# Performance work log

Hardware: AMD Instinct MI355X
Metric: run time of the kernel (lower is better)

## Reference

```python
import jax, jax.numpy as jnp
import numpy as np

NUM_GRAPHS = 3000
L = 7        # num_gc_layers
D = 256      # dims * power
DIMS = 64
POWER = 4
MSG_EPS = 1e-7
LN_EPS = 1e-5


def layer_norm(x, g, b):
    mu = jnp.mean(x, axis=-1, keepdims=True)
    var = jnp.var(x, axis=-1, keepdims=True)
    return (x - mu) * jax.lax.rsqrt(var + LN_EPS) * g + b


def gen_conv(h, src, dst, edge_emb, w, b, n_nodes):
    # GENConv (OGB DeeperGCN), aggr='add', mlp_layers=1:
    #   msg = relu(x_j + e) + eps ; agg = scatter_add ; out = Linear(x + agg)
    msg = jax.nn.relu(h[src] + edge_emb) + MSG_EPS      # [E, D]
    agg = jax.ops.segment_sum(msg, dst, num_segments=n_nodes)
    return (h + agg) @ w + b


def mlp_vn(v, w1, b1, g1, be1, w2, b2, g2, be2):
    # MLP([D, D, D], norm='layer'): Lin -> LN -> ReLU -> Lin -> LN -> ReLU
    v = jax.nn.relu(layer_norm(v @ w1 + b1, g1, be1))
    v = jax.nn.relu(layer_norm(v @ w2 + b2, g2, be2))
    return v


def _forward(x, edge_attr, edge_index, batch, atom_emb, bond_emb, vn_emb,
             gcn_w, gcn_b, norm_g, norm_b, ffn_w, ffn_b,
             vn_w1, vn_b1, vn_g1, vn_be1, vn_w2, vn_b2, vn_g2, vn_be2):
    N = x.shape[0]
    # AtomEncoder / BondEncoder: sum of per-feature embedding gathers
    h = atom_emb[jnp.arange(9), x].sum(axis=1)              # [N, D]
    edge_emb = bond_emb[jnp.arange(3), edge_attr].sum(axis=1)  # [E, D]
    h_init = h

    vn = jnp.broadcast_to(vn_emb[0], (NUM_GRAPHS, D))        # Embedding(1, D) row 0
    h = h + vn[batch]

    src, dst = edge_index[0], edge_index[1]
    out = []
    h = gen_conv(h, src, dst, edge_emb, gcn_w[0], gcn_b[0], N)
    out.append(h @ ffn_w[0] + ffn_b[0])

    for layer in range(1, L):
        h2 = jax.nn.relu(layer_norm(h, norm_g[layer - 1], norm_b[layer - 1]))
        vn_tmp = jax.ops.segment_sum(h2, batch, num_segments=NUM_GRAPHS) + vn
        j = layer - 1
        vn = mlp_vn(vn_tmp, vn_w1[j], vn_b1[j], vn_g1[j], vn_be1[j],
                    vn_w2[j], vn_b2[j], vn_g2[j], vn_be2[j])  # dropout: eval mode -> identity
        h2 = h2 + vn[batch]
        h = gen_conv(h2, src, dst, edge_emb, gcn_w[layer], gcn_b[layer], N) + h
        out.append(h @ ffn_w[layer] + ffn_b[layer])

    h_graph = jnp.concatenate([out[p] for p in range(POWER)], axis=-1)  # [N, 4*64]
    return h_graph, h_init


def setup_inputs() -> dict:
    key = jax.random.key(0)
    ks = jax.random.split(key, 12)
    N, E = 100000, 300000
    s = 0.05
    return dict(
        x=jax.random.randint(ks[0], (N, 9), 0, 64),
        edge_attr=jax.random.randint(ks[1], (E, 3), 0, 8),
        edge_index=jax.random.randint(ks[2], (2, E), 0, N),
        batch=jnp.sort(jax.random.randint(ks[3], (N,), 0, NUM_GRAPHS)),
        atom_emb=jax.random.normal(ks[4], (9, 64, D)) * s,
        bond_emb=jax.random.normal(ks[5], (3, 8, D)) * s,
        vn_emb=jnp.zeros((1, D)),
        gcn_w=jax.random.normal(ks[6], (L, D, D)) * s,
        gcn_b=jnp.zeros((L, D)),
        norm_g=jnp.ones((L, D)),
        norm_b=jnp.zeros((L, D)),
        ffn_w=jax.random.normal(ks[7], (L, D, DIMS)) * s,
        ffn_b=jnp.zeros((L, DIMS)),
        vn_w1=jax.random.normal(ks[8], (L - 1, D, D)) * s,
        vn_b1=jnp.zeros((L - 1, D)),
        vn_g1=jnp.ones((L - 1, D)),
        vn_be1=jnp.zeros((L - 1, D)),
        vn_w2=jax.random.normal(ks[9], (L - 1, D, D)) * s,
        vn_b2=jnp.zeros((L - 1, D)),
        vn_g2=jnp.ones((L - 1, D)),
        vn_be2=jnp.zeros((L - 1, D)),
    )


def reference(x, edge_attr, edge_index, batch, atom_emb, bond_emb, vn_emb,
              gcn_w, gcn_b, norm_g, norm_b, ffn_w, ffn_b,
              vn_w1, vn_b1, vn_g1, vn_be1, vn_w2, vn_b2, vn_g2, vn_be2):
    return _forward(x, edge_attr, edge_index, batch, atom_emb, bond_emb, vn_emb,
                    gcn_w, gcn_b, norm_g, norm_b, ffn_w, ffn_b,
                    vn_w1, vn_b1, vn_g1, vn_be1, vn_w2, vn_b2, vn_g2, vn_be2)
```

## Files before the change

kernel.cpp:

```cpp
#include <hip/hip_runtime.h>
#include <hip/hip_bf16.h>

#define G_NUM 3000

typedef unsigned short u16;
typedef unsigned int u32;

typedef short s16x8 __attribute__((ext_vector_type(8)));
typedef float f32x4 __attribute__((ext_vector_type(4)));

__device__ __forceinline__ float bf2f(u16 u) {
    union { u32 i; float f; } v; v.i = ((u32)u) << 16; return v.f;
}
__device__ __forceinline__ u16 f2bf(float f) {
    union { float f; u32 i; } v; v.f = f;
    u32 r = (v.i + 0x7FFFu + ((v.i >> 16) & 1u)) >> 16;
    return (u16)r;
}
__device__ __forceinline__ float ldf(const void* p, size_t i, int bf) {
    return bf ? bf2f(((const u16*)p)[i]) : ((const float*)p)[i];
}

__device__ __forceinline__ void gl_lds16(const void* g, void* l) {
    __builtin_amdgcn_global_load_lds(
        (const __attribute__((address_space(1))) void*)g,
        (__attribute__((address_space(3))) void*)l, 16, 0, 0);
}

__global__ void k_flag(const u32* __restrict__ norm_g_u32, int* __restrict__ flag) {
    if (threadIdx.x == 0 && blockIdx.x == 0)
        *flag = (norm_g_u32[0] == 0x3F803F80u) ? 1 : 0;
}

__global__ void k_hist(const int* __restrict__ ei, int* __restrict__ cnt, int E) {
    int e = blockIdx.x * blockDim.x + threadIdx.x;
    if (e < E) atomicAdd(&cnt[ei[E + e]], 1);
}

__global__ __launch_bounds__(256) void k_scan_part(const int* __restrict__ cnt,
                                                   int* __restrict__ epos,
                                                   int* __restrict__ part, int N) {
    __shared__ int sh[256];
    int t = threadIdx.x;
    int base = blockIdx.x * 1024 + t * 4;
    int c0 = (base + 0 < N) ? cnt[base + 0] : 0;
    int c1 = (base + 1 < N) ? cnt[base + 1] : 0;
    int c2 = (base + 2 < N) ? cnt[base + 2] : 0;
    int c3 = (base + 3 < N) ? cnt[base + 3] : 0;
    int s4 = c0 + c1 + c2 + c3;
    sh[t] = s4;
    __syncthreads();
    for (int off = 1; off < 256; off <<= 1) {
        int v = (t >= off) ? sh[t - off] : 0;
        __syncthreads();
        sh[t] += v;
        __syncthreads();
    }
    int excl = sh[t] - s4;
    if (base + 0 < N) epos[base + 0] = excl;
    if (base + 1 < N) epos[base + 1] = excl + c0;
    if (base + 2 < N) epos[base + 2] = excl + c0 + c1;
    if (base + 3 < N) epos[base + 3] = excl + c0 + c1 + c2;
    if (t == 255) part[blockIdx.x] = sh[255];
}

__global__ __launch_bounds__(256) void k_scan_top(int* __restrict__ part, int NB) {
    __shared__ int sh[256];
    int t = threadIdx.x;
    int v = (t < NB) ? part[t] : 0;
    sh[t] = v;
    __syncthreads();
    for (int off = 1; off < 256; off <<= 1) {
        int u = (t >= off) ? sh[t - off] : 0;
        __syncthreads();
        sh[t] += u;
        __syncthreads();
    }
    if (t < NB) part[t] = sh[t] - v;
}

__global__ __launch_bounds__(256) void k_scan_fin(int* __restrict__ epos,
                                                  const int* __restrict__ part, int N) {
    int add = part[blockIdx.x];
    int base = blockIdx.x * 1024 + threadIdx.x * 4;
#pragma unroll
    for (int i = 0; i < 4; ++i)
        if (base + i < N) epos[base + i] += add;
}

__global__ void k_scatter(const int* __restrict__ ei, int* __restrict__ epos,
                          int* __restrict__ elist, int E) {
    int e = blockIdx.x * blockDim.x + threadIdx.x;
    if (e < E) {
        int p = atomicAdd(&epos[ei[E + e]], 1);
        elist[p] = e;
    }
}

__global__ void k_atom(const int* __restrict__ x, const void* __restrict__ atom_emb,
                       const void* __restrict__ vn_emb, const int* __restrict__ flagp,
                       float* __restrict__ h, int N) {
    int id = blockIdx.x * blockDim.x + threadIdx.x;
    if (id >= N * 64) return;
    int bf = *flagp;
    int n = id >> 6, d = (id & 63) << 2;
    float s0 = 0.f, s1 = 0.f, s2 = 0.f, s3 = 0.f;
#pragma unroll
    for (int f = 0; f < 9; ++f) {
        size_t row = (size_t)(f * 64 + x[n * 9 + f]) * 256 + d;
        if (bf) {
            ushort4 v = *(const ushort4*)((const u16*)atom_emb + row);
            s0 += bf2f(v.x); s1 += bf2f(v.y); s2 += bf2f(v.z); s3 += bf2f(v.w);
        } else {
            float4 v = *(const float4*)((const float*)atom_emb + row);
            s0 += v.x; s1 += v.y; s2 += v.z; s3 += v.w;
        }
    }
    float4 o = { s0 + ldf(vn_emb, d, bf),     s1 + ldf(vn_emb, d + 1, bf),
                 s2 + ldf(vn_emb, d + 2, bf), s3 + ldf(vn_emb, d + 3, bf) };
    *(float4*)(h + (size_t)n * 256 + d) = o;
}

__global__ void k_hinit(const int* __restrict__ x, const void* __restrict__ atom_emb,
                        const int* __restrict__ flagp, void* __restrict__ d_out_v, int N) {
    int id = blockIdx.x * blockDim.x + threadIdx.x;
    if (id >= N * 64) return;
    int bf = *flagp;
    int n = id >> 6, d = (id & 63) << 2;
    float s0 = 0.f, s1 = 0.f, s2 = 0.f, s3 = 0.f;
#pragma unroll
    for (int f = 0; f < 9; ++f) {
        size_t row = (size_t)(f * 64 + x[n * 9 + f]) * 256 + d;
        if (bf) {
            ushort4 v = *(const ushort4*)((const u16*)atom_emb + row);
            s0 += bf2f(v.x); s1 += bf2f(v.y); s2 += bf2f(v.z); s3 += bf2f(v.w);
        } else {
            float4 v = *(const float4*)((const float*)atom_emb + row);
            s0 += v.x; s1 += v.y; s2 += v.z; s3 += v.w;
        }
    }
    size_t idx = (size_t)N * 256 + (size_t)n * 256 + d;
    if (bf) {
        ushort4 o = { f2bf(s0), f2bf(s1), f2bf(s2), f2bf(s3) };
        *(ushort4*)((u16*)d_out_v + idx) = o;
    } else {
        float4 o = { s0, s1, s2, s3 };
        *(float4*)((float*)d_out_v + idx) = o;
    }
}

__global__ void k_init_vn(const void* __restrict__ vn_emb, const int* __restrict__ flagp,
                          float* __restrict__ vn) {
    int id = blockIdx.x * blockDim.x + threadIdx.x;
    if (id >= G_NUM * 256) return;
    vn[id] = ldf(vn_emb, id & 255, *flagp);
}

__global__ __launch_bounds__(256) void k_agg(
    const int* __restrict__ ei, const int* __restrict__ eattr,
    const int* __restrict__ elist, const int* __restrict__ epos,
    const int* __restrict__ cnt, const void* __restrict__ bond_emb,
    const int* __restrict__ flagp, const float* __restrict__ h,
    const void* __restrict__ d_out_v, u16* __restrict__ xh, u16* __restrict__ xl,
    const float* __restrict__ vnarr, const int* __restrict__ batch,
    int layer0, int E, int N) {
    int bf = *flagp;
    int wv = threadIdx.x >> 6, lane = threadIdx.x & 63;
    int n = blockIdx.x * 4 + wv;
    if (n >= N) return;
    int d = lane << 2;
    size_t ND = (size_t)N * 256;
    const u16* h2p = (const u16*)d_out_v + (bf ? ND : 2 * ND);
    int end = epos[n];
    int deg = cnt[n];
    int start = end - deg;

    float i0, i1, i2, i3;
    if (layer0) {
        float4 iv = *(const float4*)(h + (size_t)n * 256 + d);
        i0 = iv.x; i1 = iv.y; i2 = iv.z; i3 = iv.w;
    } else {
        float4 vv = *(const float4*)(vnarr + (size_t)batch[n] * 256 + d);
        ushort4 iv = *(const ushort4*)(h2p + (size_t)n * 256 + d);
        i0 = bf2f(iv.x) + vv.x; i1 = bf2f(iv.y) + vv.y;
        i2 = bf2f(iv.z) + vv.z; i3 = bf2f(iv.w) + vv.w;
    }

    float a0 = 0.f, a1 = 0.f, a2 = 0.f, a3 = 0.f;
    for (int b0i = 0; b0i < deg; b0i += 64) {
        int m = min(64, deg - b0i);
        int src = 0, bsrc = 0, c0 = 0, c1 = 0, c2 = 0;
        if (lane < m) {
            int e = elist[start + b0i + lane];
            src = ei[e];
            c0 = eattr[e * 3]; c1 = eattr[e * 3 + 1]; c2 = eattr[e * 3 + 2];
            if (!layer0) bsrc = batch[src];
        }
        for (int j = 0; j < m; ++j) {
            int sj = __shfl(src, j);
            int q0 = __shfl(c0, j), q1 = __shfl(c1, j), q2 = __shfl(c2, j);
            float e0, e1, e2, e3;
            if (bf) {
                const u16* bp = (const u16*)bond_emb;
                ushort4 w0 = *(const ushort4*)(bp + (size_t)q0 * 256 + d);
                ushort4 w1 = *(const ushort4*)(bp + (size_t)(8 + q1) * 256 + d);
                ushort4 w2 = *(const ushort4*)(bp + (size_t)(16 + q2) * 256 + d);
                e0 = bf2f(w0.x) + bf2f(w1.x) + bf2f(w2.x);
                e1 = bf2f(w0.y) + bf2f(w1.y) + bf2f(w2.y);
                e2 = bf2f(w0.z) + bf2f(w1.z) + bf2f(w2.z);
                e3 = bf2f(w0.w) + bf2f(w1.w) + bf2f(w2.w);
            } else {
                const float* bp = (const float*)bond_emb;
                float4 w0 = *(const float4*)(bp + (size_t)q0 * 256 + d);
                float4 w1 = *(const float4*)(bp + (size_t)(8 + q1) * 256 + d);
                float4 w2 = *(const float4*)(bp + (size_t)(16 + q2) * 256 + d);
                e0 = w0.x + w1.x + w2.x; e1 = w0.y + w1.y + w2.y;
                e2 = w0.z + w1.z + w2.z; e3 = w0.w + w1.w + w2.w;
            }
            float h0, h1, h2v, h3;
            if (layer0) {
                float4 hs = *(const float4*)(h + (size_t)sj * 256 + d);
                h0 = hs.x; h1 = hs.y; h2v = hs.z; h3 = hs.w;
            } else {
                int bj = __shfl(bsrc, j);
                float4 vv = *(const float4*)(vnarr + (size_t)bj * 256 + d);
                ushort4 hs = *(const ushort4*)(h2p + (size_t)sj * 256 + d);
                h0 = bf2f(hs.x) + vv.x; h1 = bf2f(hs.y) + vv.y;
                h2v = bf2f(hs.z) + vv.z; h3 = bf2f(hs.w) + vv.w;
            }
            a0 += fmaxf(h0 + e0, 0.f) + 1e-7f;
            a1 += fmaxf(h1 + e1, 0.f) + 1e-7f;
            a2 += fmaxf(h2v + e2, 0.f) + 1e-7f;
            a3 += fmaxf(h3 + e3, 0.f) + 1e-7f;
        }
    }

    float o0 = i0 + a0, o1 = i1 + a1, o2 = i2 + a2, o3 = i3 + a3;
    u16 h0 = f2bf(o0), h1 = f2bf(o1), h2 = f2bf(o2), h3 = f2bf(o3);
    ushort4 hv = { h0, h1, h2, h3 };
    size_t base = (size_t)n * 256 + d;
    *(ushort4*)(xh + base) = hv;
    if (!bf) {
        ushort4 lv = { f2bf(o0 - bf2f(h0)), f2bf(o1 - bf2f(h1)),
                       f2bf(o2 - bf2f(h2)), f2bf(o3 - bf2f(h3)) };
        *(ushort4*)(xl + base) = lv;
    }
}

__global__ void k_prep_w(const void* __restrict__ gcn_w, const void* __restrict__ ffn_w,
                         const int* __restrict__ flagp,
                         u16* __restrict__ cwh, u16* __restrict__ cwl,
                         u16* __restrict__ fwh, u16* __restrict__ fwl) {
    int bf = *flagp;
    int t = blockIdx.x * blockDim.x + threadIdx.x;
    const int CONVT = 4 * 8 * 16 * 64;
    const int FFNT  = 4 * 8 * 4 * 64;
    if (t >= CONVT + FFNT) return;
    bool isc = t < CONVT;
    int u = isc ? t : t - CONVT;
    int lane = u & 63;
    int g = lane >> 4, c16 = lane & 15;
    int ncf = isc ? 16 : 4;
    int fid = u >> 6;
    int cf = fid % ncf;
    int kk = (fid / ncf) & 7;
    int layer = fid / (ncf * 8);
    int ncol = isc ? 256 : 64;
    int col = cf * 16 + c16;
    const void* W = isc ? gcn_w : ffn_w;
    u16* oh = isc ? cwh : fwh;
    u16* ol = isc ? cwl : fwl;
    size_t lbase = (size_t)layer * 256 * ncol;
    size_t o = (size_t)u * 8;
#pragma unroll
    for (int i = 0; i < 8; ++i) {
        int k = kk * 32 + g * 8 + i;
        float v = ldf(W, lbase + (size_t)k * ncol + col, bf);
        u16 hv = f2bf(v);
        oh[o + i] = hv;
        ol[o + i] = f2bf(v - bf2f(hv));
    }
}

__global__ __launch_bounds__(512, 8) void k_mconv(
    const u16* __restrict__ Ah, const u16* __restrict__ Al,
    const u16* __restrict__ cwh, const u16* __restrict__ cwl,
    const u16* __restrict__ fwh, const u16* __restrict__ fwl,
    const void* __restrict__ cbias, const void* __restrict__ fbias,
    const void* __restrict__ res, void* __restrict__ hOut,
    void* __restrict__ d_out_v, const int* __restrict__ flagp,
    const void* __restrict__ ng, const void* __restrict__ nb,
    int cboff, int fboff, int col_off, int goff, int N) {
    __shared__ __align__(16) u16 Shi[32 * 256];
    __shared__ __align__(16) u16 Slo[32 * 256];
    __shared__ float redS[8][2][16];
    __shared__ float redQ[8][2][16];
    int bf = *flagp;
    int t = threadIdx.x;
    int wv = t >> 6, lane = t & 63;
    int g = lane >> 4, c16 = lane & 15;
    int r0 = blockIdx.x * 32;
    size_t ND = (size_t)N * 256;
    u16* h2p = (u16*)d_out_v + (bf ? ND : 2 * ND);

    {
        int l5 = lane >> 5;
        int cb = (lane & 31) * 16;
#pragma unroll
        for (int j = 0; j < 2; ++j) {
            int rowl = wv * 4 + j * 2 + l5;
            int gr = r0 + rowl; if (gr > N - 1) gr = N - 1;
            int scb = cb ^ ((rowl & 7) << 4);
            const u16* sh = Ah + (size_t)gr * 256 + (scb >> 1);
            gl_lds16(sh, &Shi[wv * 1024 + j * 512]);
            if (!bf) {
                const u16* sl = Al + (size_t)gr * 256 + (scb >> 1);
                gl_lds16(sl, &Slo[wv * 1024 + j * 512]);
            }
        }
    }
    __syncthreads();

    f32x4 acc[2][2] = {};
    if (bf) {
#pragma unroll
        for (int kk = 0; kk < 8; ++kk) {
            s16x8 wh[2];
#pragma unroll
            for (int c = 0; c < 2; ++c)
                wh[c] = *(const s16x8*)(cwh + ((size_t)((kk * 16 + wv * 2 + c) * 64 + lane) * 8));
#pragma unroll
            for (int rf = 0; rf < 2; ++rf) {
                int R = rf * 16 + c16;
                int cbyte = (kk * 64 + g * 16) ^ ((R & 7) << 4);
                s16x8 ah = *(const s16x8*)((const char*)Shi + R * 512 + cbyte);
#pragma unroll
                for (int c = 0; c < 2; ++c)
                    acc[rf][c] = __builtin_amdgcn_mfma_f32_16x16x32_bf16(wh[c], ah, acc[rf][c], 0, 0, 0);
            }
        }
    } else {
#pragma unroll
        for (int kk = 0; kk < 8; ++kk) {
            s16x8 wh[2], wl[2];
#pragma unroll
            for (int c = 0; c < 2; ++c) {
                size_t off = (size_t)((kk * 16 + wv * 2 + c) * 64 + lane) * 8;
                wh[c] = *(const s16x8*)(cwh + off);
                wl[c] = *(const s16x8*)(cwl + off);
            }
#pragma unroll
            for (int rf = 0; rf < 2; ++rf) {
                int R = rf * 16 + c16;
                int cbyte = (kk * 64 + g * 16) ^ ((R & 7) << 4);
                s16x8 ah = *(const s16x8*)((const char*)Shi + R * 512 + cbyte);
                s16x8 al = *(const s16x8*)((const char*)Slo + R * 512 + cbyte);
#pragma unroll
                for (int c = 0; c < 2; ++c) {
                    acc[rf][c] = __builtin_amdgcn_mfma_f32_16x16x32_bf16(wh[c], ah, acc[rf][c], 0, 0, 0);
                    acc[rf][c] = __builtin_amdgcn_mfma_f32_16x16x32_bf16(wh[c], al, acc[rf][c], 0, 0, 0);
                    acc[rf][c] = __builtin_amdgcn_mfma_f32_16x16x32_bf16(wl[c], ah, acc[rf][c], 0, 0, 0);
                }
            }
        }
    }
    __syncthreads();

    float o[2][2][4];
#pragma unroll
    for (int rf = 0; rf < 2; ++rf) {
        int R = rf * 16 + c16;
        int r = r0 + R;
#pragma unroll
        for (int c = 0; c < 2; ++c) {
            int colb = (wv * 2 + c) * 16 + g * 4;
#pragma unroll
            for (int i = 0; i < 4; ++i)
                o[rf][c][i] = acc[rf][c][i] + ldf(cbias, cboff + colb + i, bf);
            if (res && r < N) {
                if (bf) {
                    ushort4 rv = *(const ushort4*)((const u16*)res + (size_t)r * 256 + colb);
                    o[rf][c][0] += bf2f(rv.x); o[rf][c][1] += bf2f(rv.y);
                    o[rf][c][2] += bf2f(rv.z); o[rf][c][3] += bf2f(rv.w);
                } else {
                    float4 rv = *(const float4*)((const float*)res + (size_t)r * 256 + colb);
                    o[rf][c][0] += rv.x; o[rf][c][1] += rv.y;
                    o[rf][c][2] += rv.z; o[rf][c][3] += rv.w;
                }
            }
        }
        if (hOut && r < N) {
#pragma unroll
            for (int c = 0; c < 2; ++c) {
                int colb = (wv * 2 + c) * 16 + g * 4;
                if (bf) {
                    ushort4 ov = { f2bf(o[rf][c][0]), f2bf(o[rf][c][1]),
                                   f2bf(o[rf][c][2]), f2bf(o[rf][c][3]) };
                    *(ushort4*)((u16*)hOut + (size_t)r * 256 + colb) = ov;
                } else {
                    float4 ov = { o[rf][c][0], o[rf][c][1], o[rf][c][2], o[rf][c][3] };
                    *(float4*)((float*)hOut + (size_t)r * 256 + colb) = ov;
                }
            }
        }
    }

    float mu[2], rs_[2];
    if (goff >= 0) {
#pragma unroll
        for (int rf = 0; rf < 2; ++rf) {
            float s = 0.f;
#pragma unroll
            for (int c = 0; c < 2; ++c)
#pragma unroll
                for (int i = 0; i < 4; ++i) s += o[rf][c][i];
            s += __shfl_xor(s, 16);
            s += __shfl_xor(s, 32);
            if (g == 0) redS[wv][rf][c16] = s;
        }
    }
    __syncthreads();
    if (goff >= 0) {
#pragma unroll
        for (int rf = 0; rf < 2; ++rf) {
            float s8 = 0.f;
#pragma unroll
            for (int w = 0; w < 8; ++w) s8 += redS[w][rf][c16];
            mu[rf] = s8 * (1.f / 256.f);
            float q = 0.f;
#pragma unroll
            for (int c = 0; c < 2; ++c)
#pragma unroll
                for (int i = 0; i < 4; ++i) {
                    float dv = o[rf][c][i] - mu[rf];
                    q += dv * dv;
                }
            q += __shfl_xor(q, 16);
            q += __shfl_xor(q, 32);
            if (g == 0) redQ[wv][rf][c16] = q;
        }
    }
    __syncthreads();
    if (goff >= 0) {
#pragma unroll
        for (int rf = 0; rf < 2; ++rf) {
            float q8 = 0.f;
#pragma unroll
            for (int w = 0; w < 8; ++w) q8 += redQ[w][rf][c16];
            float var = q8 * (1.f / 256.f);
            rs_[rf] = rsqrtf(fmaxf(var, 0.f) + 1e-5f);
            int r = r0 + rf * 16 + c16;
            if (r < N) {
#pragma unroll
                for (int c = 0; c < 2; ++c) {
                    int colb = (wv * 2 + c) * 16 + g * 4;
                    float v0 = fmaxf((o[rf][c][0] - mu[rf]) * rs_[rf] * ldf(ng, goff + colb, bf)     + ldf(nb, goff + colb, bf), 0.f);
                    float v1 = fmaxf((o[rf][c][1] - mu[rf]) * rs_[rf] * ldf(ng, goff + colb + 1, bf) + ldf(nb, goff + colb + 1, bf), 0.f);
                    float v2 = fmaxf((o[rf][c][2] - mu[rf]) * rs_[rf] * ldf(ng, goff + colb + 2, bf) + ldf(nb, goff + colb + 2, bf), 0.f);
                    float v3 = fmaxf((o[rf][c][3] - mu[rf]) * rs_[rf] * ldf(ng, goff + colb + 3, bf) + ldf(nb, goff + colb + 3, bf), 0.f);
                    ushort4 q4 = { f2bf(v0), f2bf(v1), f2bf(v2), f2bf(v3) };
                    *(ushort4*)(h2p + (size_t)r * 256 + colb) = q4;
                }
            }
        }
    }

#pragma unroll
    for (int rf = 0; rf < 2; ++rf) {
        int R = rf * 16 + c16;
#pragma unroll
        for (int c = 0; c < 2; ++c) {
            int colb = (wv * 2 + c) * 16 + g * 4;
            float o0 = o[rf][c][0], o1 = o[rf][c][1], o2 = o[rf][c][2], o3 = o[rf][c][3];
            u16 h0 = f2bf(o0), h1 = f2bf(o1), h2 = f2bf(o2), h3 = f2bf(o3);
            ushort4 hv = { h0, h1, h2, h3 };
            int cbyte = (colb * 2) ^ ((R & 7) << 4);
            *(ushort4*)((char*)Shi + R * 512 + cbyte) = hv;
            if (!bf) {
                ushort4 lv = { f2bf(o0 - bf2f(h0)), f2bf(o1 - bf2f(h1)),
                               f2bf(o2 - bf2f(h2)), f2bf(o3 - bf2f(h3)) };
                *(ushort4*)((char*)Slo + R * 512 + cbyte) = lv;
            }
        }
    }
    __syncthreads();

    f32x4 fa = {};
    {
        int rfw = wv >> 2, cfw = wv & 3;
        int R = rfw * 16 + c16;
        if (bf) {
#pragma unroll
            for (int kk = 0; kk < 8; ++kk) {
                s16x8 wh = *(const s16x8*)(fwh + ((size_t)((kk * 4 + cfw) * 64 + lane) * 8));
                int cbyte = (kk * 64 + g * 16) ^ ((R & 7) << 4);
                s16x8 ah = *(const s16x8*)((const char*)Shi + R * 512 + cbyte);
                fa = __builtin_amdgcn_mfma_f32_16x16x32_bf16(wh, ah, fa, 0, 0, 0);
            }
        } else {
#pragma unroll
            for (int kk = 0; kk < 8; ++kk) {
                size_t off = (size_t)((kk * 4 + cfw) * 64 + lane) * 8;
                s16x8 wh = *(const s16x8*)(fwh + off);
                s16x8 wl = *(const s16x8*)(fwl + off);
                int cbyte = (kk * 64 + g * 16) ^ ((R & 7) << 4);
                s16x8 ah = *(const s16x8*)((const char*)Shi + R * 512 + cbyte);
                s16x8 al = *(const s16x8*)((const char*)Slo + R * 512 + cbyte);
                fa = __builtin_amdgcn_mfma_f32_16x16x32_bf16(wh, ah, fa, 0, 0, 0);
                fa = __builtin_amdgcn_mfma_f32_16x16x32_bf16(wh, al, fa, 0, 0, 0);
                fa = __builtin_amdgcn_mfma_f32_16x16x32_bf16(wl, ah, fa, 0, 0, 0);
            }
        }

        int colb = cfw * 16 + g * 4;
        float b0 = ldf(fbias, fboff + colb, bf);
        float b1 = ldf(fbias, fboff + colb + 1, bf);
        float b2 = ldf(fbias, fboff + colb + 2, bf);
        float b3 = ldf(fbias, fboff + colb + 3, bf);
        int r = r0 + R;
        if (r < N) {
            float o0 = fa[0] + b0, o1 = fa[1] + b1;
            float o2 = fa[2] + b2, o3 = fa[3] + b3;
            size_t oi = (size_t)r * 256 + col_off + colb;
            if (bf) {
                ushort4 q = { f2bf(o0), f2bf(o1), f2bf(o2), f2bf(o3) };
                *(ushort4*)((u16*)d_out_v + oi) = q;
            } else {
                float4 q = { o0, o1, o2, o3 };
                *(float4*)((float*)d_out_v + oi) = q;
            }
        }
    }
}

__global__ __launch_bounds__(256) void k_vn4(
    const void* __restrict__ d_out_v, const int* __restrict__ flagp,
    const int* __restrict__ batch,
    const void* __restrict__ w1, const void* __restrict__ b1,
    const void* __restrict__ g1, const void* __restrict__ be1,
    const void* __restrict__ w2, const void* __restrict__ b2,
    const void* __restrict__ g2, const void* __restrict__ be2,
    float* __restrict__ vn, int woff, int voff, int N) {
    __shared__ float row[4][256];
    __shared__ float red[4][4];
    __shared__ __align__(16) float Ws[32][256];
    int bf = *flagp;
    int t = threadIdx.x;
    int wv = t >> 6, lane = t & 63;
    size_t ND = (size_t)N * 256;
    const u16* h2p = (const u16*)d_out_v + (bf ? ND : 2 * ND);

    {
        int gi = blockIdx.x * 4 + wv;
        int lo = 0, hi = N;
        while (lo < hi) { int m = (lo + hi) >> 1; if (batch[m] < gi) lo = m + 1; else hi = m; }
        int s = lo; hi = N;
        while (lo < hi) { int m = (lo + hi) >> 1; if (batch[m] < gi + 1) lo = m + 1; else hi = m; }
        int e = lo;
        int d = lane << 2;
        float4 a = *(const float4*)(vn + (size_t)gi * 256 + d);
        for (int n = s; n < e; ++n) {
            ushort4 hv = *(const ushort4*)(h2p + (size_t)n * 256 + d);
            a.x += bf2f(hv.x); a.y += bf2f(hv.y); a.z += bf2f(hv.z); a.w += bf2f(hv.w);
        }
        *(float4*)&row[wv][d] = a;
    }
    __syncthreads();

#pragma unroll 1
    for (int stage = 0; stage < 2; ++stage) {
        const void* W = stage ? w2 : w1;
        const void* B = stage ? b2 : b1;
        const void* G = stage ? g2 : g1;
        const void* BE = stage ? be2 : be1;
        float bb = ldf(B, voff + t, bf);
        float acc[4] = { bb, bb, bb, bb };
#pragma unroll 1
        for (int k0 = 0; k0 < 256; k0 += 32) {
            if (bf) {
                const u32* Wg = (const u32*)((const u16*)W + woff);
#pragma unroll
                for (int i = 0; i < 16; ++i) {
                    int idx = t + i * 256;
                    int k = idx >> 7, c2 = idx & 127;
                    u32 v = Wg[(size_t)(k0 + k) * 128 + c2];
                    Ws[k][2 * c2] = bf2f((u16)(v & 0xffff));
                    Ws[k][2 * c2 + 1] = bf2f((u16)(v >> 16));
                }
            } else {
                const float4* Wg = (const float4*)((const float*)W + woff);
#pragma unroll
                for (int i = 0; i < 8; ++i) {
                    int idx = t + i * 256;
                    int k = idx >> 6, c4 = idx & 63;
                    *(float4*)&Ws[k][4 * c4] = Wg[(size_t)(k0 + k) * 64 + c4];
                }
            }
            __syncthreads();
#pragma unroll
            for (int k = 0; k < 32; ++k) {
                float w = Ws[k][t];
                float r0 = row[0][k0 + k], r1 = row[1][k0 + k];
                float r2 = row[2][k0 + k], r3 = row[3][k0 + k];
                acc[0] = fmaf(r0, w, acc[0]);
                acc[1] = fmaf(r1, w, acc[1]);
                acc[2] = fmaf(r2, w, acc[2]);
                acc[3] = fmaf(r3, w, acc[3]);
            }
            __syncthreads();
        }
        float mu[4], rs_[4];
#pragma unroll
        for (int gr = 0; gr < 4; ++gr) {
            float s = acc[gr];
#pragma unroll
            for (int o = 32; o > 0; o >>= 1) s += __shfl_xor(s, o);
            if (lane == 0) red[wv][gr] = s;
        }
        __syncthreads();
#pragma unroll
        for (int gr = 0; gr < 4; ++gr)
            mu[gr] = (red[0][gr] + red[1][gr] + red[2][gr] + red[3][gr]) * (1.f / 256.f);
        __syncthreads();
#pragma unroll
        for (int gr = 0; gr < 4; ++gr) {
            float dv = acc[gr] - mu[gr];
            float q = dv * dv;
#pragma unroll
            for (int o = 32; o > 0; o >>= 1) q += __shfl_xor(q, o);
            if (lane == 0) red[wv][gr] = q;
        }
        __syncthreads();
        float gn = ldf(G, voff + t, bf), bn = ldf(BE, voff + t, bf);
#pragma unroll
        for (int gr = 0; gr < 4; ++gr) {
            float var = (red[0][gr] + red[1][gr] + red[2][gr] + red[3][gr]) * (1.f / 256.f);
            rs_[gr] = rsqrtf(fmaxf(var, 0.f) + 1e-5f);
        }
        __syncthreads();
#pragma unroll
        for (int gr = 0; gr < 4; ++gr)
            row[gr][t] = fmaxf((acc[gr] - mu[gr]) * rs_[gr] * gn + bn, 0.f);
        __syncthreads();
    }
#pragma unroll
    for (int gr = 0; gr < 4; ++gr)
        vn[(size_t)(blockIdx.x * 4 + gr) * 256 + t] = row[gr][t];
}

extern "C" void kernel_launch(void* const* d_in, const int* in_sizes, int n_in,
                              void* d_out, int out_size, void* d_ws, size_t ws_size,
                              hipStream_t stream) {
    const int* x      = (const int*)d_in[0];
    const int* eattr  = (const int*)d_in[1];
    const int* ei     = (const int*)d_in[2];
    const int* batch  = (const int*)d_in[3];
    const void* atom_emb = d_in[4];
    const void* bond_emb = d_in[5];
    const void* vn_emb   = d_in[6];
    const void* gcn_w    = d_in[7];
    const void* gcn_b    = d_in[8];
    const void* norm_g   = d_in[9];
    const void* norm_b   = d_in[10];
    const void* ffn_w    = d_in[11];
    const void* ffn_b    = d_in[12];
    const void* vn_w1    = d_in[13];
    const void* vn_b1    = d_in[14];
    const void* vn_g1    = d_in[15];
    const void* vn_be1   = d_in[16];
    const void* vn_w2    = d_in[17];
    const void* vn_b2    = d_in[18];
    const void* vn_g2    = d_in[19];
    const void* vn_be2   = d_in[20];

    int N = in_sizes[3];
    int E = in_sizes[2] / 2;
    size_t ND = (size_t)N * 256;
    int NB = (N + 1023) / 1024;

    char* wp = (char*)d_ws;
    int*   flag   = (int*)wp;               wp += 256;
    int*   part   = (int*)wp;               wp += 1024 * 4;
    int*   cnt    = (int*)wp;               wp += (size_t)N * 4;
    int*   epos   = (int*)wp;               wp += (size_t)N * 4;
    int*   elist  = (int*)wp;               wp += (size_t)E * 4;
    float* vn     = (float*)wp;             wp += (size_t)G_NUM * 256 * 4;
    float* vn_tmp = (float*)wp;             wp += (size_t)G_NUM * 256 * 4;
    float* h      = (float*)wp;             wp += ND * 4;
    u16*   xh     = (u16*)wp;
    u16*   xl     = xh + ND;
    (void)vn_tmp;

    size_t wbytes = ((size_t)4 * 65536 * 2 + (size_t)4 * 16384 * 2) * 2;
    size_t wtop   = (ws_size - wbytes) & ~(size_t)255;
    u16* cwh = (u16*)((char*)d_ws + wtop);
    u16* cwl = cwh + (size_t)4 * 65536;
    u16* fwh = cwl + (size_t)4 * 65536;
    u16* fwl = fwh + (size_t)4 * 16384;

    int gE  = (E + 255) / 256;
    int gN4 = (N + 3) / 4;
    int gNv = (N * 64 + 255) / 256;
    int gb  = (N + 31) / 32;

    k_flag<<<1, 64, 0, stream>>>((const u32*)norm_g, flag);
    k_prep_w<<<160, 256, 0, stream>>>(gcn_w, ffn_w, flag, cwh, cwl, fwh, fwl);

    hipMemsetAsync(cnt, 0, (size_t)N * 4, stream);
    k_hist<<<gE, 256, 0, stream>>>(ei, cnt, E);
    k_scan_part<<<NB, 256, 0, stream>>>(cnt, epos, part, N);
    k_scan_top<<<1, 256, 0, stream>>>(part, NB);
    k_scan_fin<<<NB, 256, 0, stream>>>(epos, part, N);
    k_scatter<<<gE, 256, 0, stream>>>(ei, epos, elist, E);

    k_atom<<<gNv, 256, 0, stream>>>(x, atom_emb, vn_emb, flag, h, N);
    k_init_vn<<<(G_NUM * 256 + 255) / 256, 256, 0, stream>>>(vn_emb, flag, vn);

    k_agg<<<gN4, 256, 0, stream>>>(ei, eattr, elist, epos, cnt, bond_emb, flag,
                                   h, d_out, xh, xl, vn, batch, 1, E, N);
    k_mconv<<<gb, 512, 0, stream>>>(xh, xl, cwh, cwl, fwh, fwl, gcn_b, ffn_b,
                                    nullptr, h, d_out, flag, norm_g, norm_b,
                                    0, 0, 0, 0, N);

    for (int l = 1; l < 4; ++l) {
        int j = l - 1;
        k_vn4<<<G_NUM / 4, 256, 0, stream>>>(d_out, flag, batch,
                                             vn_w1, vn_b1, vn_g1, vn_be1,
                                             vn_w2, vn_b2, vn_g2, vn_be2,
                                             vn, j * 65536, j * 256, N);
        k_agg<<<gN4, 256, 0, stream>>>(ei, eattr, elist, epos, cnt, bond_emb, flag,
                                       h, d_out, xh, xl, vn, batch, 0, E, N);
        k_mconv<<<gb, 512, 0, stream>>>(xh, xl, cwh + (size_t)l * 65536,
                                        cwl + (size_t)l * 65536,
                                        fwh + (size_t)l * 16384,
                                        fwl + (size_t)l * 16384,
                                        gcn_b, ffn_b, h,
                                        (l < 3) ? h : nullptr,
                                        d_out, flag, norm_g, norm_b,
                                        l * 256, l * 64, l * 64,
                                        (l < 3) ? l * 256 : -1, N);
    }
    k_hinit<<<gNv, 256, 0, stream>>>(x, atom_emb, flag, d_out, N);
}
```

Baseline: 1.496 ms.

## Restructure conv epilogue into row-per-wave pass with shuffle-only LayerNorm

The bias-added matmul result is first staged in shared memory. Each wave then handles whole rows with contiguous per-lane columns: it adds the residual, writes the output, and computes the LayerNorm. Mean and variance come from a single-pass sum and sum-of-squares reduced only with wave shuffles, which replaces the two shared-memory reductions and their barriers and makes the residual and output accesses coalesced. In exchange it adds one extra barrier and an LDS round trip. It also changes numerics: the bias-added value is rounded to bf16 before the residual is added in bf16 mode, and E[x²]-mu² is less numerically stable than the two-pass variance.

```diff
diff --git a/kernel.cpp b/kernel.cpp
--- a/kernel.cpp
+++ b/kernel.cpp
@@ -293,8 +293,6 @@
     int cboff, int fboff, int col_off, int goff, int N) {
     __shared__ __align__(16) u16 Shi[32 * 256];
     __shared__ __align__(16) u16 Slo[32 * 256];
-    __shared__ float redS[8][2][16];
-    __shared__ float redQ[8][2][16];
     int bf = *flagp;
     int t = threadIdx.x;
     int wv = t >> 6, lane = t & 63;
@@ -366,112 +364,16 @@
     }
     __syncthreads();
 
-    float o[2][2][4];
 #pragma unroll
     for (int rf = 0; rf < 2; ++rf) {
         int R = rf * 16 + c16;
-        int r = r0 + R;
 #pragma unroll
         for (int c = 0; c < 2; ++c) {
             int colb = (wv * 2 + c) * 16 + g * 4;
-#pragma unroll
-            for (int i = 0; i < 4; ++i)
-                o[rf][c][i] = acc[rf][c][i] + ldf(cbias, cboff + colb + i, bf);
-            if (res && r < N) {
-                if (bf) {
-                    ushort4 rv = *(const ushort4*)((const u16*)res + (size_t)r * 256 + colb);
-                    o[rf][c][0] += bf2f(rv.x); o[rf][c][1] += bf2f(rv.y);
-                    o[rf][c][2] += bf2f(rv.z); o[rf][c][3] += bf2f(rv.w);
-                } else {
-                    float4 rv = *(const float4*)((const float*)res + (size_t)r * 256 + colb);
-                    o[rf][c][0] += rv.x; o[rf][c][1] += rv.y;
-                    o[rf][c][2] += rv.z; o[rf][c][3] += rv.w;
-                }
-            }
-        }
-        if (hOut && r < N) {
-#pragma unroll
-            for (int c = 0; c < 2; ++c) {
-                int colb = (wv * 2 + c) * 16 + g * 4;
-                if (bf) {
-                    ushort4 ov = { f2bf(o[rf][c][0]), f2bf(o[rf][c][1]),
-                                   f2bf(o[rf][c][2]), f2bf(o[rf][c][3]) };
-                    *(ushort4*)((u16*)hOut + (size_t)r * 256 + colb) = ov;
-                } else {
-                    float4 ov = { o[rf][c][0], o[rf][c][1], o[rf][c][2], o[rf][c][3] };
-                    *(float4*)((float*)hOut + (size_t)r * 256 + colb) = ov;
-                }
-            }
-        }
-    }
-
-    float mu[2], rs_[2];
-    if (goff >= 0) {
-#pragma unroll
-        for (int rf = 0; rf < 2; ++rf) {
-            float s = 0.f;
-#pragma unroll
-            for (int c = 0; c < 2; ++c)
-#pragma unroll
-                for (int i = 0; i < 4; ++i) s += o[rf][c][i];
-            s += __shfl_xor(s, 16);
-            s += __shfl_xor(s, 32);
-            if (g == 0) redS[wv][rf][c16] = s;
-        }
-    }
-    __syncthreads();
-    if (goff >= 0) {
-#pragma unroll
-        for (int rf = 0; rf < 2; ++rf) {
-            float s8 = 0.f;
-#pragma unroll
-            for (int w = 0; w < 8; ++w) s8 += redS[w][rf][c16];
-            mu[rf] = s8 * (1.f / 256.f);
-            float q = 0.f;
-#pragma unroll
-            for (int c = 0; c < 2; ++c)
-#pragma unroll
-                for (int i = 0; i < 4; ++i) {
-                    float dv = o[rf][c][i] - mu[rf];
-                    q += dv * dv;
-                }
-            q += __shfl_xor(q, 16);
-            q += __shfl_xor(q, 32);
-            if (g == 0) redQ[wv][rf][c16] = q;
-        }
-    }
-    __syncthreads();
-    if (goff >= 0) {
-#pragma unroll
-        for (int rf = 0; rf < 2; ++rf) {
-            float q8 = 0.f;
-#pragma unroll
-            for (int w = 0; w < 8; ++w) q8 += redQ[w][rf][c16];
-            float var = q8 * (1.f / 256.f);
-            rs_[rf] = rsqrtf(fmaxf(var, 0.f) + 1e-5f);
-            int r = r0 + rf * 16 + c16;
-            if (r < N) {
-#pragma unroll
-                for (int c = 0; c < 2; ++c) {
-                    int colb = (wv * 2 + c) * 16 + g * 4;
-                    float v0 = fmaxf((o[rf][c][0] - mu[rf]) * rs_[rf] * ldf(ng, goff + colb, bf)     + ldf(nb, goff + colb, bf), 0.f);
-                    float v1 = fmaxf((o[rf][c][1] - mu[rf]) * rs_[rf] * ldf(ng, goff + colb + 1, bf) + ldf(nb, goff + colb + 1, bf), 0.f);
-                    float v2 = fmaxf((o[rf][c][2] - mu[rf]) * rs_[rf] * ldf(ng, goff + colb + 2, bf) + ldf(nb, goff + colb + 2, bf), 0.f);
-                    float v3 = fmaxf((o[rf][c][3] - mu[rf]) * rs_[rf] * ldf(ng, goff + colb + 3, bf) + ldf(nb, goff + colb + 3, bf), 0.f);
-                    ushort4 q4 = { f2bf(v0), f2bf(v1), f2bf(v2), f2bf(v3) };
-                    *(ushort4*)(h2p + (size_t)r * 256 + colb) = q4;
-                }
-            }
-        }
-    }
-
-#pragma unroll
-    for (int rf = 0; rf < 2; ++rf) {
-        int R = rf * 16 + c16;
-#pragma unroll
-        for (int c = 0; c < 2; ++c) {
-            int colb = (wv * 2 + c) * 16 + g * 4;
-            float o0 = o[rf][c][0], o1 = o[rf][c][1], o2 = o[rf][c][2], o3 = o[rf][c][3];
+            float o0 = acc[rf][c][0] + ldf(cbias, cboff + colb, bf);
+            float o1 = acc[rf][c][1] + ldf(cbias, cboff + colb + 1, bf);
+            float o2 = acc[rf][c][2] + ldf(cbias, cboff + colb + 2, bf);
+            float o3 = acc[rf][c][3] + ldf(cbias, cboff + colb + 3, bf);
             u16 h0 = f2bf(o0), h1 = f2bf(o1), h2 = f2bf(o2), h3 = f2bf(o3);
             ushort4 hv = { h0, h1, h2, h3 };
             int cbyte = (colb * 2) ^ ((R & 7) << 4);
@@ -480,6 +382,70 @@
                 ushort4 lv = { f2bf(o0 - bf2f(h0)), f2bf(o1 - bf2f(h1)),
                                f2bf(o2 - bf2f(h2)), f2bf(o3 - bf2f(h3)) };
                 *(ushort4*)((char*)Slo + R * 512 + cbyte) = lv;
+            }
+        }
+    }
+    __syncthreads();
+
+#pragma unroll
+    for (int pass = 0; pass < 4; ++pass) {
+        int row = wv + pass * 8;
+        int r = r0 + row;
+        bool valid = r < N;
+        int sb = (lane * 8) ^ ((row & 7) << 4);
+        ushort4 hq = *(const ushort4*)((const char*)Shi + row * 512 + sb);
+        float v0 = bf2f(hq.x), v1 = bf2f(hq.y), v2 = bf2f(hq.z), v3 = bf2f(hq.w);
+        if (!bf) {
+            ushort4 lq = *(const ushort4*)((const char*)Slo + row * 512 + sb);
+            v0 += bf2f(lq.x); v1 += bf2f(lq.y); v2 += bf2f(lq.z); v3 += bf2f(lq.w);
+        }
+        if (res && valid) {
+            if (bf) {
+                ushort4 rv = *(const ushort4*)((const u16*)res + (size_t)r * 256 + lane * 4);
+                v0 += bf2f(rv.x); v1 += bf2f(rv.y); v2 += bf2f(rv.z); v3 += bf2f(rv.w);
+            } else {
+                float4 rv = *(const float4*)((const float*)res + (size_t)r * 256 + lane * 4);
+                v0 += rv.x; v1 += rv.y; v2 += rv.z; v3 += rv.w;
+            }
+        }
+        if (hOut && valid) {
+            if (bf) {
+                ushort4 ov = { f2bf(v0), f2bf(v1), f2bf(v2), f2bf(v3) };
+                *(ushort4*)((u16*)hOut + (size_t)r * 256 + lane * 4) = ov;
+            } else {
+                float4 ov = { v0, v1, v2, v3 };
+                *(float4*)((float*)hOut + (size_t)r * 256 + lane * 4) = ov;
+            }
+        }
+        if (goff >= 0) {
+            float s = v0 + v1 + v2 + v3;
+            float q = v0 * v0 + v1 * v1 + v2 * v2 + v3 * v3;
+#pragma unroll
+            for (int o = 32; o > 0; o >>= 1) {
+                s += __shfl_xor(s, o);
+                q += __shfl_xor(q, o);
+            }
+            float mu = s * (1.f / 256.f);
+            float var = q * (1.f / 256.f) - mu * mu;
+            float rs = rsqrtf(fmaxf(var, 0.f) + 1e-5f);
+            int d4 = lane * 4;
+            float w0 = fmaxf((v0 - mu) * rs * ldf(ng, goff + d4, bf)     + ldf(nb, goff + d4, bf), 0.f);
+            float w1 = fmaxf((v1 - mu) * rs * ldf(ng, goff + d4 + 1, bf) + ldf(nb, goff + d4 + 1, bf), 0.f);
+            float w2 = fmaxf((v2 - mu) * rs * ldf(ng, goff + d4 + 2, bf) + ldf(nb, goff + d4 + 2, bf), 0.f);
+            float w3 = fmaxf((v3 - mu) * rs * ldf(ng, goff + d4 + 3, bf) + ldf(nb, goff + d4 + 3, bf), 0.f);
+            if (valid) {
+                ushort4 q4 = { f2bf(w0), f2bf(w1), f2bf(w2), f2bf(w3) };
+                *(ushort4*)(h2p + (size_t)r * 256 + d4) = q4;
+            }
+        }
+        if (res) {
+            u16 a0 = f2bf(v0), a1 = f2bf(v1), a2 = f2bf(v2), a3 = f2bf(v3);
+            ushort4 hv = { a0, a1, a2, a3 };
+            *(ushort4*)((char*)Shi + row * 512 + sb) = hv;
+            if (!bf) {
+                ushort4 lv = { f2bf(v0 - bf2f(a0)), f2bf(v1 - bf2f(a1)),
+                               f2bf(v2 - bf2f(a2)), f2bf(v3 - bf2f(a3)) };
+                *(ushort4*)((char*)Slo + row * 512 + sb) = lv;
             }
         }
     }
```

After: 1.547 ms. 1.03x slower.
